# Optimization experiments

Hardware: AMD Instinct MI355X
Metric: run time of the kernel (lower is better)

The kernel has to match this reference:

```python
import jax, jax.numpy as jnp
import numpy as np

N_NODES = 50000
N_EDGES = 800000
IN_DIM = 256
HID = [256, 128]
NEG_SLOPE = 0.01  # F.leaky_relu default


def setup_inputs() -> dict:
    key = jax.random.key(0)
    ks = jax.random.split(key, 8)
    x = jax.random.normal(ks[0], (N_NODES, IN_DIM), dtype=jnp.float32)
    w1 = jax.random.normal(ks[1], (IN_DIM, HID[0]), dtype=jnp.float32) * (1.0 / np.sqrt(IN_DIM))
    b1 = jnp.zeros((HID[0],), dtype=jnp.float32)
    w2 = jax.random.normal(ks[2], (HID[0], HID[1]), dtype=jnp.float32) * (1.0 / np.sqrt(HID[0]))
    b2 = jnp.zeros((HID[1],), dtype=jnp.float32)
    src = jax.random.randint(ks[3], (N_EDGES,), 0, N_NODES, dtype=jnp.int32)
    dst = jax.random.randint(ks[4], (N_EDGES,), 0, N_NODES, dtype=jnp.int32)
    edge_weight = jax.random.uniform(ks[5], (N_EDGES,), dtype=jnp.float32)
    return {"x": x, "w1": w1, "b1": b1, "w2": w2, "b2": b2,
            "src": src, "dst": dst, "edge_weight": edge_weight}


def _gcn_layer(h, w, b, src, dst, ew, n_nodes):
    # GraphConvolution: support = h @ W ; out = spmm(adj, support) + b
    support = h @ w                              # [N, d_out]
    msg = support[src] * ew[:, None]             # [E, d_out] gather + scale
    agg = jax.ops.segment_sum(msg, dst, num_segments=n_nodes)  # [N, d_out]
    return agg + b


def reference(x, w1, b1, w2, b2, src, dst, edge_weight):
    # layer 1: GCN -> leaky_relu -> dropout(eval: identity)
    h = _gcn_layer(x, w1, b1, src, dst, edge_weight, N_NODES)
    h = jax.nn.leaky_relu(h, NEG_SLOPE)
    # layer 2
    h = _gcn_layer(h, w2, b2, src, dst, edge_weight, N_NODES)
    h = jax.nn.leaky_relu(h, NEG_SLOPE)
    return h
```

## Files before the change

### kernel.cpp

```cpp
#include <hip/hip_runtime.h>

#define NEG_SLOPE 0.01f

constexpr int N_NODES_C = 50000;
constexpr int N_EDGES_C = 800000;
constexpr int M_PAD = 50048;

typedef short bf16x8 __attribute__((ext_vector_type(8)));
typedef float f32x4 __attribute__((ext_vector_type(4)));

__device__ inline unsigned short f2bf(float f) {
  unsigned int u = __float_as_uint(f);
  u += 0x7FFF + ((u >> 16) & 1);
  return (unsigned short)(u >> 16);
}
__device__ inline float bf2f(unsigned int h16) {
  return __uint_as_float(h16 << 16);
}


__global__ __launch_bounds__(256) void histogram_kernel(const int* __restrict__ dst,
                                                        int* __restrict__ counts) {
  int e = blockIdx.x * 256 + threadIdx.x;
  if (e < N_EDGES_C) atomicAdd(&counts[dst[e]], 1);
}

constexpr int N_SCAN_BLKS = (N_NODES_C + 255) / 256;

__global__ __launch_bounds__(256) void scan_phase_a(const int* __restrict__ counts,
                                                    int* __restrict__ partial,
                                                    int* __restrict__ blk_sums) {
  __shared__ int s[256];
  const int t = threadIdx.x;
  const int i = blockIdx.x * 256 + t;
  const int v = (i < N_NODES_C) ? counts[i] : 0;
  s[t] = v;
  __syncthreads();
  for (int off = 1; off < 256; off <<= 1) {
    int u = (t >= off) ? s[t - off] : 0;
    __syncthreads();
    s[t] += u;
    __syncthreads();
  }
  if (i < N_NODES_C) partial[i] = s[t] - v;
  if (t == 255) blk_sums[blockIdx.x] = s[255];
}

__global__ __launch_bounds__(256) void scan_phase_b(const int* __restrict__ blk_sums,
                                                    int* __restrict__ blk_off) {
  __shared__ int s[256];
  const int t = threadIdx.x;
  const int v = (t < N_SCAN_BLKS) ? blk_sums[t] : 0;
  s[t] = v;
  __syncthreads();
  for (int off = 1; off < 256; off <<= 1) {
    int u = (t >= off) ? s[t - off] : 0;
    __syncthreads();
    s[t] += u;
    __syncthreads();
  }
  if (t < N_SCAN_BLKS) blk_off[t] = s[t] - v;
}

__global__ __launch_bounds__(256) void scan_phase_c(const int* __restrict__ partial,
                                                    const int* __restrict__ blk_off,
                                                    int* __restrict__ row_ptr,
                                                    int* __restrict__ cursor) {
  const int i = blockIdx.x * 256 + threadIdx.x;
  if (i < N_NODES_C) {
    const int r = partial[i] + blk_off[blockIdx.x];
    row_ptr[i] = r;
    cursor[i] = r;
  }
  if (i == 0) row_ptr[N_NODES_C] = N_EDGES_C;
}

__global__ __launch_bounds__(256) void fill_kernel(const int* __restrict__ src,
                                                   const int* __restrict__ dst,
                                                   const float* __restrict__ ew,
                                                   int* __restrict__ cursor,
                                                   uint2* __restrict__ s_meta) {
  int e = blockIdx.x * 256 + threadIdx.x;
  if (e < N_EDGES_C) {
    int p = atomicAdd(&cursor[dst[e]], 1);
    uint2 m;
    m.x = (unsigned)src[e];
    m.y = __float_as_uint(ew[e]);
    s_meta[p] = m;
  }
}


__global__ __launch_bounds__(256) void conv_x_kernel(const float* __restrict__ x,
                                                     unsigned short* __restrict__ xb) {
  int idx = blockIdx.x * 256 + threadIdx.x;
  if (idx >= M_PAD * 32) return;
  int row = idx >> 5;
  int c8 = (idx & 31) << 3;
  uint4 v;
  if (row < N_NODES_C) {
    const float4* p = (const float4*)(x + (size_t)row * 256 + c8);
    float4 a = p[0], b = p[1];
    v.x = f2bf(a.x) | ((unsigned)f2bf(a.y) << 16);
    v.y = f2bf(a.z) | ((unsigned)f2bf(a.w) << 16);
    v.z = f2bf(b.x) | ((unsigned)f2bf(b.y) << 16);
    v.w = f2bf(b.z) | ((unsigned)f2bf(b.w) << 16);
  } else {
    v = make_uint4(0, 0, 0, 0);
  }
  *(uint4*)(xb + (size_t)row * 256 + c8) = v;
}

__global__ __launch_bounds__(256) void conv_wT_kernel(const float* __restrict__ w,
                                                      unsigned short* __restrict__ wT,
                                                      int K, int N) {
  int idx = blockIdx.x * 256 + threadIdx.x;
  if (idx >= K * N) return;
  int n = idx / K, k = idx - n * K;
  wT[idx] = f2bf(w[(size_t)k * N + n]);
}


#define GLOAD_LDS16(g, l)                                              \
  __builtin_amdgcn_global_load_lds(                                    \
      (__attribute__((address_space(1))) void*)(g),                    \
      (__attribute__((address_space(3))) void*)(l), 16, 0, 0)

__global__ __launch_bounds__(256) void gemm_bf16_kernel(
    const unsigned short* __restrict__ A,
    const unsigned short* __restrict__ BT,
    unsigned short* __restrict__ C,
    int N) {
  constexpr int K = 256;
  __shared__ short Asm[128 * 32];
  __shared__ short Bsm[128 * 32];
  const int tid = threadIdx.x;
  const int lane = tid & 63, wave = tid >> 6;
  const int wm = wave & 1, wn = wave >> 1;
  const int row0 = blockIdx.y * 128, col0 = blockIdx.x * 128;

  const int ch0 = wave * 2, ch1 = wave * 2 + 1;
  const int o0 = ch0 * 512 + lane * 8;
  const int o1 = ch1 * 512 + lane * 8;
  const int r0 = o0 >> 5, c0 = o0 & 31;
  const int r1 = o1 >> 5, c1 = o1 & 31;

  f32x4 acc[4][4] = {};

  for (int k0 = 0; k0 < K; k0 += 32) {
    GLOAD_LDS16(A + (size_t)(row0 + r0) * K + k0 + c0, &Asm[ch0 * 512]);
    GLOAD_LDS16(A + (size_t)(row0 + r1) * K + k0 + c1, &Asm[ch1 * 512]);
    GLOAD_LDS16(BT + (size_t)(col0 + r0) * K + k0 + c0, &Bsm[ch0 * 512]);
    GLOAD_LDS16(BT + (size_t)(col0 + r1) * K + k0 + c1, &Bsm[ch1 * 512]);
    __builtin_amdgcn_s_waitcnt(0);
    __syncthreads();

    bf16x8 af[4], bf[4];
#pragma unroll
    for (int mt = 0; mt < 4; ++mt)
      af[mt] = *(const bf16x8*)&Asm[(wm * 64 + mt * 16 + (lane & 15)) * 32 + (lane >> 4) * 8];
#pragma unroll
    for (int nt = 0; nt < 4; ++nt)
      bf[nt] = *(const bf16x8*)&Bsm[(wn * 64 + nt * 16 + (lane & 15)) * 32 + (lane >> 4) * 8];
#pragma unroll
    for (int mt = 0; mt < 4; ++mt)
#pragma unroll
      for (int nt = 0; nt < 4; ++nt)
        acc[mt][nt] = __builtin_amdgcn_mfma_f32_16x16x32_bf16(af[mt], bf[nt], acc[mt][nt], 0, 0, 0);
    __syncthreads();
  }

  const int cl = lane & 15, rq = (lane >> 4) * 4;
#pragma unroll
  for (int mt = 0; mt < 4; ++mt) {
    const int rbase = row0 + wm * 64 + mt * 16 + rq;
#pragma unroll
    for (int nt = 0; nt < 4; ++nt) {
      const int col = col0 + wn * 64 + nt * 16 + cl;
#pragma unroll
      for (int i = 0; i < 4; ++i)
        C[(size_t)(rbase + i) * N + col] = f2bf(acc[mt][nt][i]);
    }
  }
}


template <int D, bool OUT_BF16>
__global__ __launch_bounds__(256) void agg_kernel(
    const unsigned short* __restrict__ support, const uint2* __restrict__ s_meta,
    const int* __restrict__ row_ptr, const float* __restrict__ bias,
    unsigned short* __restrict__ out_bf, float* __restrict__ out_f, int n_total) {
  constexpr int G = D / 8;
  constexpr int EPW = 64 / G;
  const int lane = threadIdx.x & 63;
  const int sub = lane / G;
  const int li = lane % G;
  const int n = blockIdx.x * 4 + (threadIdx.x >> 6);
  if (n >= n_total) return;
  const bool valid = n < N_NODES_C;

  float acc[8] = {};

  if (valid) {
    const int start = row_ptr[n];
    const int end = row_ptr[n + 1];
    for (int j0 = start; j0 < end; j0 += 64) {
      const int cnt = min(64, end - j0);
      int e = 0;
      float w = 0.f;
      if (lane < cnt) {
        uint2 m = s_meta[j0 + lane];
        e = (int)m.x;
        w = __uint_as_float(m.y);
      }
      const int nIter = (cnt + EPW - 1) / EPW;
#pragma unroll 8
      for (int c = 0; c < nIter; ++c) {
        const int slot = c * EPW + sub;
        const int s = __shfl(e, slot);
        const float wt = __shfl(w, slot);
        uint4 v = *(const uint4*)(support + (size_t)s * D + li * 8);
        acc[0] += bf2f(v.x & 0xffffu) * wt;
        acc[1] += bf2f(v.x >> 16) * wt;
        acc[2] += bf2f(v.y & 0xffffu) * wt;
        acc[3] += bf2f(v.y >> 16) * wt;
        acc[4] += bf2f(v.z & 0xffffu) * wt;
        acc[5] += bf2f(v.z >> 16) * wt;
        acc[6] += bf2f(v.w & 0xffffu) * wt;
        acc[7] += bf2f(v.w >> 16) * wt;
      }
    }
  }

#pragma unroll
  for (int j = 0; j < 8; ++j) {
    acc[j] += __shfl_xor(acc[j], 32);
    if (G == 16) acc[j] += __shfl_xor(acc[j], 16);
  }

  if (OUT_BF16) {
    if (sub == 0) {
      unsigned short o[8];
#pragma unroll
      for (int j = 0; j < 8; ++j) {
        if (valid) {
          float v = acc[j] + bias[li * 8 + j];
          v = v >= 0.f ? v : NEG_SLOPE * v;
          o[j] = f2bf(v);
        } else {
          o[j] = 0;
        }
      }
      uint4 pk;
      pk.x = o[0] | ((unsigned)o[1] << 16);
      pk.y = o[2] | ((unsigned)o[3] << 16);
      pk.z = o[4] | ((unsigned)o[5] << 16);
      pk.w = o[6] | ((unsigned)o[7] << 16);
      *(uint4*)(out_bf + (size_t)n * D + li * 8) = pk;
    }
  } else {
    if (valid && sub == 0) {
      float r[8];
#pragma unroll
      for (int j = 0; j < 8; ++j) {
        float v = acc[j] + bias[li * 8 + j];
        r[j] = v >= 0.f ? v : NEG_SLOPE * v;
      }
      *(float4*)(out_f + (size_t)n * D + li * 8) = make_float4(r[0], r[1], r[2], r[3]);
      *(float4*)(out_f + (size_t)n * D + li * 8 + 4) = make_float4(r[4], r[5], r[6], r[7]);
    }
  }
}


extern "C" void kernel_launch(void* const* d_in, const int* in_sizes, int n_in,
                              void* d_out, int out_size, void* d_ws, size_t ws_size,
                              hipStream_t stream) {
  const float* x  = (const float*)d_in[0];
  const float* w1 = (const float*)d_in[1];
  const float* b1 = (const float*)d_in[2];
  const float* w2 = (const float*)d_in[3];
  const float* b2 = (const float*)d_in[4];
  const int*   src = (const int*)d_in[5];
  const int*   dst = (const int*)d_in[6];
  const float* ew  = (const float*)d_in[7];
  float* out = (float*)d_out;

  unsigned short* xb   = (unsigned short*)d_ws;
  unsigned short* a2b  = xb + (size_t)M_PAD * 256;
  unsigned short* sup1 = a2b + (size_t)M_PAD * 256;
  unsigned short* sup2 = sup1 + (size_t)M_PAD * 256;
  unsigned short* w1T  = sup2 + (size_t)M_PAD * 128;
  unsigned short* w2T  = w1T + 256 * 256;
  int* counts  = (int*)(w2T + 128 * 256);
  int* cursor  = counts + N_NODES_C;
  int* row_ptr = cursor + N_NODES_C;
  int* partial = row_ptr + (N_NODES_C + 1);
  int* blk_sums= partial + N_NODES_C;
  int* blk_off = blk_sums + 256;
  uint2* s_meta = (uint2*)(blk_off + 256 + 2);

  const int EB = (N_EDGES_C + 255) / 256;

  hipMemsetAsync(counts, 0, N_NODES_C * sizeof(int), stream);
  histogram_kernel<<<EB, 256, 0, stream>>>(dst, counts);
  scan_phase_a<<<N_SCAN_BLKS, 256, 0, stream>>>(counts, partial, blk_sums);
  scan_phase_b<<<1, 256, 0, stream>>>(blk_sums, blk_off);
  scan_phase_c<<<N_SCAN_BLKS, 256, 0, stream>>>(partial, blk_off, row_ptr, cursor);
  fill_kernel<<<EB, 256, 0, stream>>>(src, dst, ew, cursor, s_meta);

  conv_x_kernel<<<(M_PAD * 32 + 255) / 256, 256, 0, stream>>>(x, xb);
  conv_wT_kernel<<<(256 * 256 + 255) / 256, 256, 0, stream>>>(w1, w1T, 256, 256);
  conv_wT_kernel<<<(128 * 256 + 255) / 256, 256, 0, stream>>>(w2, w2T, 256, 128);

  gemm_bf16_kernel<<<dim3(2, M_PAD / 128), 256, 0, stream>>>(xb, w1T, sup1, 256);
  agg_kernel<256, true><<<M_PAD / 4, 256, 0, stream>>>(sup1, s_meta, row_ptr,
                                                       b1, a2b, nullptr, M_PAD);

  gemm_bf16_kernel<<<dim3(1, M_PAD / 128), 256, 0, stream>>>(a2b, w2T, sup2, 128);
  agg_kernel<128, false><<<N_NODES_C / 4, 256, 0, stream>>>(sup2, s_meta, row_ptr,
                                                            b2, nullptr, out, N_NODES_C);
}
```

Before: 327.1 us.

## Slice GEMM output by feature columns and aggregate per slice for cache locality

```diff
diff --git a/kernel.cpp b/kernel.cpp
--- a/kernel.cpp
+++ b/kernel.cpp
@@ -18,11 +18,47 @@
   return __uint_as_float(h16 << 16);
 }
 
-
-__global__ __launch_bounds__(256) void histogram_kernel(const int* __restrict__ dst,
-                                                        int* __restrict__ counts) {
-  int e = blockIdx.x * 256 + threadIdx.x;
-  if (e < N_EDGES_C) atomicAdd(&counts[dst[e]], 1);
+constexpr int NB_CONVX = (M_PAD * 32) / 256;
+constexpr int NB_W1 = (256 * 256) / 256;
+constexpr int NB_W2 = (256 * 128) / 256;
+constexpr int NB_HIST = N_EDGES_C / 256;
+constexpr int NB_PRE = NB_CONVX + NB_W1 + NB_W2 + NB_HIST;
+
+__global__ __launch_bounds__(256) void pre_kernel(
+    const float* __restrict__ x, const float* __restrict__ w1,
+    const float* __restrict__ w2, const int* __restrict__ dst,
+    unsigned short* __restrict__ xb, unsigned short* __restrict__ w1T,
+    unsigned short* __restrict__ w2T, int* __restrict__ counts) {
+  const int bx = blockIdx.x;
+  const int tid = threadIdx.x;
+  if (bx < NB_CONVX) {
+    int idx = bx * 256 + tid;
+    int row = idx >> 5;
+    int c8 = (idx & 31) << 3;
+    uint4 v;
+    if (row < N_NODES_C) {
+      const float4* p = (const float4*)(x + (size_t)row * 256 + c8);
+      float4 a = p[0], b = p[1];
+      v.x = f2bf(a.x) | ((unsigned)f2bf(a.y) << 16);
+      v.y = f2bf(a.z) | ((unsigned)f2bf(a.w) << 16);
+      v.z = f2bf(b.x) | ((unsigned)f2bf(b.y) << 16);
+      v.w = f2bf(b.z) | ((unsigned)f2bf(b.w) << 16);
+    } else {
+      v = make_uint4(0, 0, 0, 0);
+    }
+    *(uint4*)(xb + (size_t)row * 256 + c8) = v;
+  } else if (bx < NB_CONVX + NB_W1) {
+    int idx = (bx - NB_CONVX) * 256 + tid;
+    int n = idx >> 8, k = idx & 255;
+    w1T[idx] = f2bf(w1[(size_t)k * 256 + n]);
+  } else if (bx < NB_CONVX + NB_W1 + NB_W2) {
+    int idx = (bx - NB_CONVX - NB_W1) * 256 + tid;
+    int n = idx >> 8, k = idx & 255;
+    w2T[idx] = f2bf(w2[(size_t)k * 128 + n]);
+  } else {
+    int e = (bx - NB_CONVX - NB_W1 - NB_W2) * 256 + tid;
+    atomicAdd(&counts[dst[e]], 1);
+  }
 }
 
 constexpr int N_SCAN_BLKS = (N_NODES_C + 255) / 256;
@@ -91,36 +127,6 @@
 }
 
 
-__global__ __launch_bounds__(256) void conv_x_kernel(const float* __restrict__ x,
-                                                     unsigned short* __restrict__ xb) {
-  int idx = blockIdx.x * 256 + threadIdx.x;
-  if (idx >= M_PAD * 32) return;
-  int row = idx >> 5;
-  int c8 = (idx & 31) << 3;
-  uint4 v;
-  if (row < N_NODES_C) {
-    const float4* p = (const float4*)(x + (size_t)row * 256 + c8);
-    float4 a = p[0], b = p[1];
-    v.x = f2bf(a.x) | ((unsigned)f2bf(a.y) << 16);
-    v.y = f2bf(a.z) | ((unsigned)f2bf(a.w) << 16);
-    v.z = f2bf(b.x) | ((unsigned)f2bf(b.y) << 16);
-    v.w = f2bf(b.z) | ((unsigned)f2bf(b.w) << 16);
-  } else {
-    v = make_uint4(0, 0, 0, 0);
-  }
-  *(uint4*)(xb + (size_t)row * 256 + c8) = v;
-}
-
-__global__ __launch_bounds__(256) void conv_wT_kernel(const float* __restrict__ w,
-                                                      unsigned short* __restrict__ wT,
-                                                      int K, int N) {
-  int idx = blockIdx.x * 256 + threadIdx.x;
-  if (idx >= K * N) return;
-  int n = idx / K, k = idx - n * K;
-  wT[idx] = f2bf(w[(size_t)k * N + n]);
-}
-
-
 #define GLOAD_LDS16(g, l)                                              \
   __builtin_amdgcn_global_load_lds(                                    \
       (__attribute__((address_space(1))) void*)(g),                    \
@@ -177,49 +183,45 @@
 #pragma unroll
     for (int nt = 0; nt < 4; ++nt) {
       const int col = col0 + wn * 64 + nt * 16 + cl;
+      const size_t sbase = ((size_t)(col >> 5) * M_PAD) * 32 + (col & 31);
 #pragma unroll
       for (int i = 0; i < 4; ++i)
-        C[(size_t)(rbase + i) * N + col] = f2bf(acc[mt][nt][i]);
+        C[sbase + (size_t)(rbase + i) * 32] = f2bf(acc[mt][nt][i]);
     }
   }
 }
 
 
-template <int D, bool OUT_BF16>
-__global__ __launch_bounds__(256) void agg_kernel(
-    const unsigned short* __restrict__ support, const uint2* __restrict__ s_meta,
-    const int* __restrict__ row_ptr, const float* __restrict__ bias,
-    unsigned short* __restrict__ out_bf, float* __restrict__ out_f, int n_total) {
-  constexpr int G = D / 8;
-  constexpr int EPW = 64 / G;
+template <int NSLICE, int OUT_D, bool OUT_BF16>
+__global__ __launch_bounds__(256) void agg_sliced_kernel(
+    const unsigned short* __restrict__ supS,
+    const uint2* __restrict__ s_meta, const int* __restrict__ row_ptr,
+    const float* __restrict__ bias, unsigned short* __restrict__ out_bf,
+    float* __restrict__ out_f, int n_total) {
+  const int bx = blockIdx.x;
+  const int slice = bx & (NSLICE - 1);
+  const int group = bx / NSLICE;
   const int lane = threadIdx.x & 63;
-  const int sub = lane / G;
-  const int li = lane % G;
-  const int n = blockIdx.x * 4 + (threadIdx.x >> 6);
+  const int n = group * 4 + (threadIdx.x >> 6);
   if (n >= n_total) return;
   const bool valid = n < N_NODES_C;
+
+  const int dimg = lane & 3;
+  const int slot = lane >> 2;
+  const unsigned short* tab = supS + (size_t)slice * M_PAD * 32;
 
   float acc[8] = {};
 
   if (valid) {
     const int start = row_ptr[n];
     const int end = row_ptr[n + 1];
-    for (int j0 = start; j0 < end; j0 += 64) {
-      const int cnt = min(64, end - j0);
-      int e = 0;
-      float w = 0.f;
-      if (lane < cnt) {
-        uint2 m = s_meta[j0 + lane];
-        e = (int)m.x;
-        w = __uint_as_float(m.y);
-      }
-      const int nIter = (cnt + EPW - 1) / EPW;
-#pragma unroll 8
-      for (int c = 0; c < nIter; ++c) {
-        const int slot = c * EPW + sub;
-        const int s = __shfl(e, slot);
-        const float wt = __shfl(w, slot);
-        uint4 v = *(const uint4*)(support + (size_t)s * D + li * 8);
+    for (int j = start; j < end; j += 16) {
+      const int idx = j + slot;
+      if (idx < end) {
+        uint2 m = s_meta[idx];
+        const int s = (int)m.x;
+        const float wt = __uint_as_float(m.y);
+        uint4 v = *(const uint4*)(tab + (size_t)s * 32 + dimg * 8);
         acc[0] += bf2f(v.x & 0xffffu) * wt;
         acc[1] += bf2f(v.x >> 16) * wt;
         acc[2] += bf2f(v.y & 0xffffu) * wt;
@@ -234,17 +236,20 @@
 
 #pragma unroll
   for (int j = 0; j < 8; ++j) {
+    acc[j] += __shfl_xor(acc[j], 4);
+    acc[j] += __shfl_xor(acc[j], 8);
+    acc[j] += __shfl_xor(acc[j], 16);
     acc[j] += __shfl_xor(acc[j], 32);
-    if (G == 16) acc[j] += __shfl_xor(acc[j], 16);
-  }
-
-  if (OUT_BF16) {
-    if (sub == 0) {
+  }
+
+  if (lane < 4) {
+    const int dbase = slice * 32 + lane * 8;
+    if (OUT_BF16) {
       unsigned short o[8];
 #pragma unroll
       for (int j = 0; j < 8; ++j) {
         if (valid) {
-          float v = acc[j] + bias[li * 8 + j];
+          float v = acc[j] + bias[dbase + j];
           v = v >= 0.f ? v : NEG_SLOPE * v;
           o[j] = f2bf(v);
         } else {
@@ -256,18 +261,16 @@
       pk.y = o[2] | ((unsigned)o[3] << 16);
       pk.z = o[4] | ((unsigned)o[5] << 16);
       pk.w = o[6] | ((unsigned)o[7] << 16);
-      *(uint4*)(out_bf + (size_t)n * D + li * 8) = pk;
-    }
-  } else {
-    if (valid && sub == 0) {
+      *(uint4*)(out_bf + (size_t)n * OUT_D + dbase) = pk;
+    } else if (valid) {
       float r[8];
 #pragma unroll
       for (int j = 0; j < 8; ++j) {
-        float v = acc[j] + bias[li * 8 + j];
+        float v = acc[j] + bias[dbase + j];
         r[j] = v >= 0.f ? v : NEG_SLOPE * v;
       }
-      *(float4*)(out_f + (size_t)n * D + li * 8) = make_float4(r[0], r[1], r[2], r[3]);
-      *(float4*)(out_f + (size_t)n * D + li * 8 + 4) = make_float4(r[4], r[5], r[6], r[7]);
+      *(float4*)(out_f + (size_t)n * OUT_D + dbase) = make_float4(r[0], r[1], r[2], r[3]);
+      *(float4*)(out_f + (size_t)n * OUT_D + dbase + 4) = make_float4(r[4], r[5], r[6], r[7]);
     }
   }
 }
@@ -303,21 +306,18 @@
   const int EB = (N_EDGES_C + 255) / 256;
 
   hipMemsetAsync(counts, 0, N_NODES_C * sizeof(int), stream);
-  histogram_kernel<<<EB, 256, 0, stream>>>(dst, counts);
+  pre_kernel<<<NB_PRE, 256, 0, stream>>>(x, w1, w2, dst, xb, w1T, w2T, counts);
+
   scan_phase_a<<<N_SCAN_BLKS, 256, 0, stream>>>(counts, partial, blk_sums);
   scan_phase_b<<<1, 256, 0, stream>>>(blk_sums, blk_off);
   scan_phase_c<<<N_SCAN_BLKS, 256, 0, stream>>>(partial, blk_off, row_ptr, cursor);
   fill_kernel<<<EB, 256, 0, stream>>>(src, dst, ew, cursor, s_meta);
 
-  conv_x_kernel<<<(M_PAD * 32 + 255) / 256, 256, 0, stream>>>(x, xb);
-  conv_wT_kernel<<<(256 * 256 + 255) / 256, 256, 0, stream>>>(w1, w1T, 256, 256);
-  conv_wT_kernel<<<(128 * 256 + 255) / 256, 256, 0, stream>>>(w2, w2T, 256, 128);
-
   gemm_bf16_kernel<<<dim3(2, M_PAD / 128), 256, 0, stream>>>(xb, w1T, sup1, 256);
-  agg_kernel<256, true><<<M_PAD / 4, 256, 0, stream>>>(sup1, s_meta, row_ptr,
-                                                       b1, a2b, nullptr, M_PAD);
+  agg_sliced_kernel<8, 256, true><<<(M_PAD / 4) * 8, 256, 0, stream>>>(
+      sup1, s_meta, row_ptr, b1, a2b, nullptr, M_PAD);
 
   gemm_bf16_kernel<<<dim3(1, M_PAD / 128), 256, 0, stream>>>(a2b, w2T, sup2, 128);
-  agg_kernel<128, false><<<N_NODES_C / 4, 256, 0, stream>>>(sup2, s_meta, row_ptr,
-                                                            b2, nullptr, out, N_NODES_C);
-}
+  agg_sliced_kernel<4, 128, false><<<((N_NODES_C + 3) / 4) * 4, 256, 0, stream>>>(
+      sup2, s_meta, row_ptr, b2, nullptr, out, N_NODES_C);
+}
```

Result: slower. 495.7 us (+51.6%).
